# Performance work log

Hardware: AMD Instinct MI355X
Metric: run time of the kernel (lower is better)

## Reference

```python
import jax, jax.numpy as jnp
import numpy as np

WS = 8            # window_size
SHIFT = WS // 2   # cyclic shift
NHEADS = 6
EPS = 1e-5


def _rel_pos_index(ws):
    coords = np.stack(np.meshgrid(np.arange(ws), np.arange(ws), indexing='ij'))  # [2,ws,ws]
    flat = coords.reshape(2, -1)                       # [2,N]
    rel = flat[:, :, None] - flat[:, None, :]          # [2,N,N]
    rel = rel.transpose(1, 2, 0).copy()
    rel[:, :, 0] += ws - 1
    rel[:, :, 1] += ws - 1
    rel[:, :, 0] *= 2 * ws - 1
    return rel.sum(-1)                                 # [N,N] indices into bias table


def _attn_mask(H, W, ws, shift):
    # standard Swin boundary mask for the shifted configuration
    img = np.zeros((H, W))
    cnt = 0
    for hs in (slice(0, -ws), slice(-ws, -shift), slice(-shift, None)):
        for wsl in (slice(0, -ws), slice(-ws, -shift), slice(-shift, None)):
            img[hs, wsl] = cnt
            cnt += 1
    mw = img.reshape(H // ws, ws, W // ws, ws).transpose(0, 2, 1, 3).reshape(-1, ws * ws)
    m = mw[:, None, :] - mw[:, :, None]
    return np.where(m != 0, -100.0, 0.0).astype(np.float32)  # [nW, N, N]


def instance_norm(x):
    # InstanceNorm over spatial dims, no affine (torch default)
    m = x.mean(axis=(2, 3), keepdims=True)
    v = x.var(axis=(2, 3), keepdims=True)
    return (x - m) * jax.lax.rsqrt(v + EPS)


def setup_inputs() -> dict:
    key = jax.random.key(0)
    ks = jax.random.split(key, 8)
    B, C, H, W, E = 4, 192, 256, 256, 128
    s = 0.02
    return {
        'x': jax.random.normal(ks[0], (B, C, H, W), jnp.float32),
        'cond': jax.random.normal(ks[1], (B, E), jnp.float32),
        'qkv_w': jax.random.normal(ks[2], (3 * C, C), jnp.float32) * s,
        'qkv_b': jnp.zeros((3 * C,), jnp.float32),
        'proj_w': jax.random.normal(ks[3], (C, C), jnp.float32) * s,
        'proj_b': jnp.zeros((C,), jnp.float32),
        'rel_bias': jax.random.normal(ks[4], ((2 * WS - 1) ** 2, NHEADS), jnp.float32) * s,
        'film_w': jax.random.normal(ks[5], (2 * C, E), jnp.float32) * s,
        'film_b': jnp.zeros((2 * C,), jnp.float32),
    }


def shifted_window_attention(xn, qkv_w, qkv_b, proj_w, proj_b, rel_bias):
    B, C, H, W = xn.shape
    h, ws, shift = NHEADS, WS, SHIFT
    d = C // h
    N = ws * ws
    nW = (H // ws) * (W // ws)
    scale = d ** -0.5

    xs = jnp.transpose(xn, (0, 2, 3, 1))                         # BHWC
    xs = jnp.roll(xs, (-shift, -shift), axis=(1, 2))             # cyclic shift
    win = xs.reshape(B, H // ws, ws, W // ws, ws, C)
    win = win.transpose(0, 1, 3, 2, 4, 5).reshape(B * nW, N, C)  # window partition

    qkv = win @ qkv_w.T + qkv_b                                  # [Bn, N, 3C]
    q, k, v = [t.reshape(B * nW, N, h, d).transpose(0, 2, 1, 3)
               for t in jnp.split(qkv, 3, axis=-1)]              # [Bn, h, N, d]

    attn = jnp.einsum('bhnd,bhmd->bhnm', q, k) * scale           # [Bn, h, N, N]
    bias = rel_bias[_rel_pos_index(ws)].transpose(2, 0, 1)       # [h, N, N]
    attn = attn + bias[None]
    mask = jnp.asarray(_attn_mask(H, W, ws, shift))              # [nW, N, N]
    attn = attn.reshape(B, nW, h, N, N) + mask[None, :, None]
    attn = jax.nn.softmax(attn, axis=-1).reshape(B * nW, h, N, N)

    out = jnp.einsum('bhnm,bhmd->bhnd', attn, v)                 # [Bn, h, N, d]
    out = out.transpose(0, 2, 1, 3).reshape(B * nW, N, C)
    out = out @ proj_w.T + proj_b

    out = out.reshape(B, H // ws, W // ws, ws, ws, C)
    out = out.transpose(0, 1, 3, 2, 4, 5).reshape(B, H, W, C)    # window merge
    out = jnp.roll(out, (shift, shift), axis=(1, 2))             # reverse shift
    return jnp.transpose(out, (0, 3, 1, 2))                      # BCHW


def reference(x, cond, qkv_w, qkv_b, proj_w, proj_b, rel_bias, film_w, film_b):
    # branch 1: x + attn(norm1(x))
    xn = instance_norm(x)
    x = x + shifted_window_attention(xn, qkv_w, qkv_b, proj_w, proj_b, rel_bias)
    # branch 2: x + FiLM(norm2(x), cond)
    x2 = instance_norm(x)
    gb = cond @ film_w.T + film_b                                # [B, 2C]
    gamma, beta = jnp.split(gb, 2, axis=-1)
    x2 = x2 * gamma[:, :, None, None] + beta[:, :, None, None]
    return x + x2
```

## Files before the change

### kernel.cpp

```cpp
#include <hip/hip_runtime.h>

#define BATCH 4
#define CH    192
#define PLANE 65536

typedef unsigned short u16;
typedef unsigned char  u8;
typedef __bf16 bf16x8_t __attribute__((ext_vector_type(8)));
typedef unsigned short u16x8 __attribute__((ext_vector_type(8)));
typedef unsigned short u16x4 __attribute__((ext_vector_type(4)));
typedef float f32x4 __attribute__((ext_vector_type(4)));

__device__ __forceinline__ u16 f2bf(float f) {
  __bf16 h = (__bf16)f;
  return __builtin_bit_cast(u16, h);
}
__device__ __forceinline__ float bf2f(u16 h) {
  unsigned u = ((unsigned)h) << 16;
  return __builtin_bit_cast(float, u);
}
__device__ __forceinline__ f32x4 mfma16(u16x8 a, u16x8 b, f32x4 c) {
  return __builtin_amdgcn_mfma_f32_16x16x32_bf16(
      __builtin_bit_cast(bf16x8_t, a), __builtin_bit_cast(bf16x8_t, b), c, 0, 0, 0);
}

__global__ void stats_kernel(const float* __restrict__ in, float* __restrict__ st) {
  const int plane = blockIdx.x;
  const float4* p = (const float4*)(in + (long)plane * PLANE);
  float s = 0.f, ss = 0.f;
  for (int i = threadIdx.x; i < PLANE/4; i += 256) {
    float4 v = p[i];
    s  += v.x + v.y + v.z + v.w;
    ss += v.x*v.x + v.y*v.y + v.z*v.z + v.w*v.w;
  }
  for (int off = 1; off < 64; off <<= 1) {
    s  += __shfl_xor(s,  off, 64);
    ss += __shfl_xor(ss, off, 64);
  }
  __shared__ float aux[4][2];
  const int w = threadIdx.x >> 6;
  if ((threadIdx.x & 63) == 0) { aux[w][0] = s; aux[w][1] = ss; }
  __syncthreads();
  if (threadIdx.x == 0) {
    float S  = aux[0][0]+aux[1][0]+aux[2][0]+aux[3][0];
    float SS = aux[0][1]+aux[1][1]+aux[2][1]+aux[3][1];
    float mean = S * (1.f/PLANE);
    float var  = SS * (1.f/PLANE) - mean*mean;
    st[plane*2]   = mean;
    st[plane*2+1] = rsqrtf(var + 1e-5f);
  }
}

__global__ void cvt_kernel(const float* __restrict__ a, const float* __restrict__ b,
                           const float* __restrict__ rb,
                           u16* __restrict__ wa, u16* __restrict__ wb, u8* __restrict__ bq) {
  const int i = blockIdx.x*256 + threadIdx.x;
  if (i < 576*192) wa[i] = f2bf(a[i]);
  if (i < 192*192) wb[i] = f2bf(b[i]);
  if (i < 1350) {
    float v = fminf(fmaxf(rintf(rb[i]*128.f) + 128.f, 0.f), 255.f);
    bq[i] = (u8)v;
  }
}

__global__ void film_prep(const float* __restrict__ cond, const float* __restrict__ fw,
                          const float* __restrict__ fb, float* __restrict__ gb) {
  const int i = blockIdx.x*256 + threadIdx.x;
  if (i >= BATCH*384) return;
  const int bb = i / 384, oc = i - bb*384;
  const float* cw = fw + oc*128;
  const float* cv = cond + bb*128;
  float s = fb[oc];
  for (int k = 0; k < 128; ++k) s += cv[k]*cw[k];
  gb[i] = s;
}

__global__ __launch_bounds__(256) void prep_kernel(
    const float* __restrict__ x, const float* __restrict__ st, u16* __restrict__ xn)
{
  __shared__ u16 tile[32*264];
  const int t = threadIdx.x;
  const int bid = blockIdx.x;
  const int cc = bid % 6;
  const int wh = (bid/6) % 32;
  const int b  = bid / 192;
  const int c0 = cc*32;
  const int ww = t >> 3, ax = t & 7;
  const int gx = (ww*8 + ax + 4) & 255;
  const int gxb = gx & ~3, gxr = gx & 3;
  const long wid = b*1024 + wh*32 + ww;

  for (int ay = 0; ay < 8; ++ay) {
    const int gy = (wh*8 + ay + 4) & 255;
    for (int it = 0; it < 8; ++it) {
      const int id = it*256 + t;
      const int cl = id >> 6;
      const int px = (id & 63) << 2;
      const int c  = c0 + cl;
      const float m = st[(b*192+c)*2], r = st[(b*192+c)*2+1];
      float4 v = *(const float4*)(x + (((long)(b*192+c)) << 16) + gy*256 + px);
      u16x4 pk;
      pk[0] = f2bf((v.x-m)*r); pk[1] = f2bf((v.y-m)*r);
      pk[2] = f2bf((v.z-m)*r); pk[3] = f2bf((v.w-m)*r);
      *(u16x4*)&tile[cl*264 + (px ^ ((cl&7)<<2))] = pk;
    }
    __syncthreads();
    u16* dst = xn + wid*12288 + (ay*8+ax)*192 + c0;
    #pragma unroll
    for (int k = 0; k < 4; ++k) {
      u16x8 pk;
      #pragma unroll
      for (int e = 0; e < 8; ++e) {
        const int c = k*8 + e;
        pk[e] = tile[c*264 + (gxb ^ ((c&7)<<2)) + gxr];
      }
      *(u16x8*)(dst + k*8) = pk;
    }
    __syncthreads();
  }
}

__global__ __launch_bounds__(512, 4) void attn_kernel(
    const u16* __restrict__ xn, const u16* __restrict__ wq, const u16* __restrict__ wp,
    const float* __restrict__ qkvb, const float* __restrict__ projb,
    const u8* __restrict__ bq, const float* __restrict__ st,
    u16* __restrict__ pw, float2* __restrict__ part)
{
  __shared__ __attribute__((aligned(16))) unsigned char smem[71504];
  u16*    Xs    = (u16*)smem;
  u16*    G     = (u16*)(smem + 25600);
  u16*    Vt    = (u16*)(smem + 43008);
  u16*    Pout  = (u16*)(smem + 25600);
  u8*     biasQ = (u8*)(smem + 52224);
  float2* stp   = (float2*)(smem + 53576);
  u16*    Ps    = (u16*)(smem + 55120);

  const int t    = threadIdx.x;
  const int lane = t & 63;
  const int wave = t >> 6;
  const int arow = lane & 15;
  const int kgrp = lane >> 4;

  const int bid = blockIdx.x;
  const int wid = (bid & 7) * 512 + (bid >> 3);
  const int b   = wid >> 10;
  const int wh  = (wid >> 5) & 31;
  const int ww  = wid & 31;

  const u16* src = xn + (long)wid*12288;
  #pragma unroll
  for (int it = 0; it < 3; ++it) {
    const int id = it*512 + t;
    const int row = id/24, c8 = (id%24)*8;
    *(u16x8*)&Xs[row*200 + c8] = *(const u16x8*)(src + id*8);
  }
  for (int i = t; i < 1350; i += 512) biasQ[i] = bq[i];
  for (int i = t; i < 192; i += 512) {
    const float mean = st[(b*192+i)*2];
    const float rstd = st[(b*192+i)*2 + 1];
    float2 o = {mean, 1.0f / rstd};
    stp[i] = o;
  }
  __syncthreads();

  const int hh = wave >> 2;
  const int mt = wave & 3;
  const bool boundary = (wh == 31) || (ww == 31);
  u16x4 og[3][2];

  #pragma unroll
  for (int g = 0; g < 3; ++g) {
    for (int nt0 = wave; nt0 < 12; nt0 += 8) {
      f32x4 acc[4] = {{0,0,0,0},{0,0,0,0},{0,0,0,0},{0,0,0,0}};
      const int col = nt0*16 + arow;
      const int mat = col >> 6;
      const int ch  = mat*192 + g*64 + (col & 63);
      const u16* wrow = wq + ch*192 + kgrp*8;
      #pragma unroll
      for (int ks = 0; ks < 6; ++ks) {
        u16x8 bfr = *(const u16x8*)(wrow + ks*32);
        #pragma unroll
        for (int m = 0; m < 4; ++m) {
          u16x8 af = *(const u16x8*)&Xs[(m*16+arow)*200 + ks*32 + kgrp*8];
          acc[m] = mfma16(af, bfr, acc[m]);
        }
      }
      const float addb = qkvb[ch];
      if (mat == 2) {
        const int vc = col & 63;
        #pragma unroll
        for (int m = 0; m < 4; ++m) {
          u16x4 pk;
          #pragma unroll
          for (int r = 0; r < 4; ++r) pk[r] = f2bf(acc[m][r] + addb);
          *(u16x4*)&Vt[vc*72 + m*16 + kgrp*4] = pk;
        }
      } else {
        const float mult = (mat == 0) ? 0.17677669529663687f : 1.0f;
        const int gc = mat*64 + (col & 63);
        #pragma unroll
        for (int m = 0; m < 4; ++m)
          #pragma unroll
          for (int r = 0; r < 4; ++r)
            G[(m*16 + kgrp*4 + r)*136 + gc] = f2bf((acc[m][r] + addb)*mult);
      }
    }
    __syncthreads();

    const int hd = g*2 + hh;
    u16x8 qf = *(const u16x8*)&G[(mt*16+arow)*136 + hh*32 + kgrp*8];
    f32x4 sv[4];
    #pragma unroll
    for (int nt = 0; nt < 4; ++nt) {
      u16x8 kf = *(const u16x8*)&G[(nt*16+arow)*136 + 64 + hh*32 + kgrp*8];
      f32x4 z = {0,0,0,0};
      sv[nt] = mfma16(qf, kf, z);
    }

    int qj6[4];
    #pragma unroll
    for (int nt = 0; nt < 4; ++nt) {
      const int j = nt*16 + arow;
      qj6[nt] = ((j>>3)*15 + (j&7))*6;
    }
    float p[4][4];
    if (!boundary) {
      #pragma unroll
      for (int r = 0; r < 4; ++r) {
        const int i = mt*16 + kgrp*4 + r;
        const int qib = ((i>>3)*15 + (i&7) + 112)*6 + hd;
        #pragma unroll
        for (int nt = 0; nt < 4; ++nt)
          p[nt][r] = sv[nt][r] + (float)((int)biasQ[qib - qj6[nt]] - 128) * 0.0078125f;
      }
    } else {
      #pragma unroll
      for (int r = 0; r < 4; ++r) {
        const int i  = mt*16 + kgrp*4 + r;
        const int iy = i >> 3, ix = i & 7;
        const int qib = (iy*15 + ix + 112)*6 + hd;
        const int ri = ((wh==31) ? (iy<4?1:2) : 0)*3 + ((ww==31) ? (ix<4?1:2) : 0);
        #pragma unroll
        for (int nt = 0; nt < 4; ++nt) {
          const int j  = nt*16 + arow;
          const int jy = j >> 3, jx = j & 7;
          const int rj = ((wh==31) ? (jy<4?1:2) : 0)*3 + ((ww==31) ? (jx<4?1:2) : 0);
          float sc = sv[nt][r] + (float)((int)biasQ[qib - qj6[nt]] - 128) * 0.0078125f;
          if (ri != rj) sc -= 100.0f;
          p[nt][r] = sc;
        }
      }
    }
    #pragma unroll
    for (int r = 0; r < 4; ++r) {
      float mx = fmaxf(fmaxf(p[0][r], p[1][r]), fmaxf(p[2][r], p[3][r]));
      for (int off = 1; off < 16; off <<= 1) mx = fmaxf(mx, __shfl_xor(mx, off, 64));
      float sum = 0.f;
      #pragma unroll
      for (int nt = 0; nt < 4; ++nt) { p[nt][r] = __expf(p[nt][r] - mx); sum += p[nt][r]; }
      for (int off = 1; off < 16; off <<= 1) sum += __shfl_xor(sum, off, 64);
      const float inv = 1.0f / sum;
      #pragma unroll
      for (int nt = 0; nt < 4; ++nt) p[nt][r] *= inv;
    }
    u16* myP = Ps + wave*1024;
    #pragma unroll
    for (int r = 0; r < 4; ++r) {
      const int i = kgrp*4 + r;
      #pragma unroll
      for (int nt = 0; nt < 4; ++nt) {
        const int j = nt*16 + arow;
        myP[i*64 + ((j + 8*i) & 63)] = f2bf(p[nt][r]);
      }
    }
    f32x4 oacc[2] = {{0,0,0,0},{0,0,0,0}};
    #pragma unroll
    for (int ks = 0; ks < 2; ++ks) {
      u16x8 pf = *(const u16x8*)&myP[arow*64 + ((ks*32 + kgrp*8 + 8*arow) & 63)];
      #pragma unroll
      for (int nt = 0; nt < 2; ++nt) {
        u16x8 vf = *(const u16x8*)&Vt[(hh*32 + nt*16 + arow)*72 + ks*32 + kgrp*8];
        oacc[nt] = mfma16(pf, vf, oacc[nt]);
      }
    }
    #pragma unroll
    for (int nt = 0; nt < 2; ++nt)
      #pragma unroll
      for (int r = 0; r < 4; ++r)
        og[g][nt][r] = f2bf(oacc[nt][r]);
    __syncthreads();
  }

  u16x8 rawreg[3];
  #pragma unroll
  for (int it = 0; it < 3; ++it) {
    const int id = it*512 + t;
    const int c = id >> 3, tk8 = (id & 7)*8;
    const float2 mi = stp[c];
    u16x8 rr;
    #pragma unroll
    for (int e = 0; e < 8; ++e) {
      float nv = bf2f(Xs[(tk8 + e)*200 + c]);
      rr[e] = f2bf(nv*mi.y + mi.x);
    }
    rawreg[it] = rr;
  }
  __syncthreads();

  #pragma unroll
  for (int g = 0; g < 3; ++g)
    #pragma unroll
    for (int nt = 0; nt < 2; ++nt) {
      const int colb = g*64 + hh*32 + nt*16 + arow;
      #pragma unroll
      for (int r = 0; r < 4; ++r)
        Xs[(mt*16 + kgrp*4 + r)*200 + colb] = og[g][nt][r];
    }
  __syncthreads();

  for (int nt0 = wave; nt0 < 12; nt0 += 8) {
    const int ch = nt0*16 + arow;
    const float pb = projb[ch];
    f32x4 acc[4];
    #pragma unroll
    for (int m = 0; m < 4; ++m) { f32x4 v = {pb,pb,pb,pb}; acc[m] = v; }
    const u16* wrow = wp + ch*192 + kgrp*8;
    #pragma unroll
    for (int ks = 0; ks < 6; ++ks) {
      u16x8 bfr = *(const u16x8*)(wrow + ks*32);
      #pragma unroll
      for (int m = 0; m < 4; ++m) {
        u16x8 af = *(const u16x8*)&Xs[(m*16+arow)*200 + ks*32 + kgrp*8];
        acc[m] = mfma16(af, bfr, acc[m]);
      }
    }
    #pragma unroll
    for (int m = 0; m < 4; ++m) {
      u16x4 pk;
      #pragma unroll
      for (int r = 0; r < 4; ++r) pk[r] = f2bf(acc[m][r]);
      *(u16x4*)&Pout[ch*72 + m*16 + kgrp*4] = pk;
    }
  }
  __syncthreads();

  u16* dstw = pw + (long)wid*12288;
  #pragma unroll
  for (int it = 0; it < 3; ++it) {
    const int id = it*512 + t;
    const int c = id >> 3, tk8 = (id & 7)*8;
    u16x8 pv = *(const u16x8*)&Pout[c*72 + tk8];
    u16x8 rr = rawreg[it];
    u16x8 vb;
    float s = 0.f, q = 0.f;
    #pragma unroll
    for (int e = 0; e < 8; ++e) {
      float v = bf2f(rr[e]) + bf2f(pv[e]);
      vb[e] = f2bf(v);
      s += v; q += v*v;
    }
    *(u16x8*)(dstw + c*64 + tk8) = vb;
    s += __shfl_xor(s, 1, 64); q += __shfl_xor(q, 1, 64);
    s += __shfl_xor(s, 2, 64); q += __shfl_xor(q, 2, 64);
    s += __shfl_xor(s, 4, 64); q += __shfl_xor(q, 4, 64);
    if ((lane & 7) == 0) {
      float2 pr = {s, q};
      part[(long)wid*192 + c] = pr;
    }
  }
}

__global__ __launch_bounds__(256) void stats2_kernel(
    const float2* __restrict__ part, float2* __restrict__ st2f) {
  const int b = blockIdx.x / 12, cg = blockIdx.x % 12;
  const int cl = threadIdx.x & 15;
  const int w0 = threadIdx.x >> 4;
  const int c = cg*16 + cl;
  float s = 0.f, q = 0.f;
  for (int w = w0; w < 1024; w += 16) {
    float2 v = part[((long)(b*1024 + w))*192 + c];
    s += v.x; q += v.y;
  }
  s += __shfl_xor(s, 16, 64); q += __shfl_xor(q, 16, 64);
  s += __shfl_xor(s, 32, 64); q += __shfl_xor(q, 32, 64);
  __shared__ float2 aux[4][16];
  if ((threadIdx.x & 63) < 16) { float2 v = {s, q}; aux[threadIdx.x >> 6][cl] = v; }
  __syncthreads();
  if (threadIdx.x < 16) {
    float2 a0 = aux[0][cl], a1 = aux[1][cl], a2 = aux[2][cl], a3 = aux[3][cl];
    float S = a0.x + a1.x + a2.x + a3.x;
    float Q = a0.y + a1.y + a2.y + a3.y;
    float mean = S * (1.f/PLANE);
    float var  = Q * (1.f/PLANE) - mean*mean;
    float2 o = {mean, rsqrtf(var + 1e-5f)};
    st2f[b*192 + c] = o;
  }
}

__global__ __launch_bounds__(256) void final_kernel(
    const u16* __restrict__ pw, const float2* __restrict__ st2f,
    const float* __restrict__ gb, float* __restrict__ out)
{
  __shared__ u16 tile[32*264];
  const int t = threadIdx.x;
  const int bid = blockIdx.x;
  const int lin = (bid & 7)*768 + (bid >> 3);
  const int cc = lin % 6;
  const int rowid = lin / 6;
  const int gy = rowid & 255;
  const int b  = rowid >> 8;
  const int c0 = cc*32;
  const int gys = (gy + 252) & 255;
  const int wh = gys >> 3, ay = gys & 7;

  {
    const int ww = t >> 3, cq = t & 7;
    const long wid = b*1024 + wh*32 + ww;
    const u16* srcw = pw + wid*12288;
    const int g1 = ww*8 + 4, g2 = (ww*8 + 8) & 255;
    #pragma unroll
    for (int j = 0; j < 4; ++j) {
      const int c = cq*4 + j;
      u16x8 v = *(const u16x8*)(srcw + (c0+c)*64 + ay*8);
      const int sw = (c & 7) << 2;
      u16x4 lo = {v[0],v[1],v[2],v[3]}, hi = {v[4],v[5],v[6],v[7]};
      *(u16x4*)&tile[c*264 + (g1 ^ sw)] = lo;
      *(u16x4*)&tile[c*264 + (g2 ^ sw)] = hi;
    }
  }
  __syncthreads();

  const int cl = t >> 3, seg = t & 7;
  const int c = c0 + cl;
  const float2 mr = st2f[b*192 + c];
  const float mean = mr.x, rstd = mr.y;
  const float gmm  = gb[b*384 + c];
  const float be   = gb[b*384 + 192 + c];
  const long base = (((long)(b*192 + c)) << 16) + gy*256 + seg*32;
  float* orow = out + base;
  const int sw = (cl & 7) << 2;
  #pragma unroll
  for (int q4 = 0; q4 < 32; q4 += 4) {
    const int px = seg*32 + q4;
    u16x4 pv = *(const u16x4*)&tile[cl*264 + (px ^ sw)];
    float4 o;
    float v0 = bf2f(pv[0]), v1 = bf2f(pv[1]), v2 = bf2f(pv[2]), v3 = bf2f(pv[3]);
    o.x = v0 + (v0 - mean)*rstd*gmm + be;
    o.y = v1 + (v1 - mean)*rstd*gmm + be;
    o.z = v2 + (v2 - mean)*rstd*gmm + be;
    o.w = v3 + (v3 - mean)*rstd*gmm + be;
    *(float4*)(orow + q4) = o;
  }
}

extern "C" void kernel_launch(void* const* d_in, const int* in_sizes, int n_in,
                              void* d_out, int out_size, void* d_ws, size_t ws_size,
                              hipStream_t stream) {
  const float* x      = (const float*)d_in[0];
  const float* cond   = (const float*)d_in[1];
  const float* qkv_w  = (const float*)d_in[2];
  const float* qkv_b  = (const float*)d_in[3];
  const float* proj_w = (const float*)d_in[4];
  const float* proj_b = (const float*)d_in[5];
  const float* relb   = (const float*)d_in[6];
  const float* film_w = (const float*)d_in[7];
  const float* film_b = (const float*)d_in[8];
  float* out = (float*)d_out;

  char* ws = (char*)d_ws;
  float*  stats1 = (float*)ws;
  float2* st2f   = (float2*)(ws + 6144);
  float*  gb     = (float*)(ws + 12288);
  u16*    wq     = (u16*)(ws + 18432);
  u16*    wp     = (u16*)(ws + 239616);
  u8*     bqq    = (u8*)(ws + 313344);
  u16*    xbuf   = (u16*)(ws + 362496);
  float2* part   = (float2*)(ws + 362496 + 100663296);

  stats_kernel<<<768, 256, 0, stream>>>(x, stats1);
  cvt_kernel<<<432, 256, 0, stream>>>(qkv_w, proj_w, relb, wq, wp, bqq);
  film_prep<<<6, 256, 0, stream>>>(cond, film_w, film_b, gb);
  prep_kernel<<<768, 256, 0, stream>>>(x, stats1, xbuf);
  attn_kernel<<<4096, 512, 0, stream>>>(xbuf, wq, wp, qkv_b, proj_b, bqq, stats1, xbuf, part);
  stats2_kernel<<<48, 256, 0, stream>>>(part, st2f);
  final_kernel<<<6144, 256, 0, stream>>>(xbuf, st2f, gb, out);
}
```

Before: 505.7 us.

## Fuse first instance-norm stats into prep pass and normalize inside attention

```diff
diff --git a/kernel.cpp b/kernel.cpp
--- a/kernel.cpp
+++ b/kernel.cpp
@@ -22,33 +22,6 @@
 __device__ __forceinline__ f32x4 mfma16(u16x8 a, u16x8 b, f32x4 c) {
   return __builtin_amdgcn_mfma_f32_16x16x32_bf16(
       __builtin_bit_cast(bf16x8_t, a), __builtin_bit_cast(bf16x8_t, b), c, 0, 0, 0);
-}
-
-__global__ void stats_kernel(const float* __restrict__ in, float* __restrict__ st) {
-  const int plane = blockIdx.x;
-  const float4* p = (const float4*)(in + (long)plane * PLANE);
-  float s = 0.f, ss = 0.f;
-  for (int i = threadIdx.x; i < PLANE/4; i += 256) {
-    float4 v = p[i];
-    s  += v.x + v.y + v.z + v.w;
-    ss += v.x*v.x + v.y*v.y + v.z*v.z + v.w*v.w;
-  }
-  for (int off = 1; off < 64; off <<= 1) {
-    s  += __shfl_xor(s,  off, 64);
-    ss += __shfl_xor(ss, off, 64);
-  }
-  __shared__ float aux[4][2];
-  const int w = threadIdx.x >> 6;
-  if ((threadIdx.x & 63) == 0) { aux[w][0] = s; aux[w][1] = ss; }
-  __syncthreads();
-  if (threadIdx.x == 0) {
-    float S  = aux[0][0]+aux[1][0]+aux[2][0]+aux[3][0];
-    float SS = aux[0][1]+aux[1][1]+aux[2][1]+aux[3][1];
-    float mean = S * (1.f/PLANE);
-    float var  = SS * (1.f/PLANE) - mean*mean;
-    st[plane*2]   = mean;
-    st[plane*2+1] = rsqrtf(var + 1e-5f);
-  }
 }
 
 __global__ void cvt_kernel(const float* __restrict__ a, const float* __restrict__ b,
@@ -76,7 +49,7 @@
 }
 
 __global__ __launch_bounds__(256) void prep_kernel(
-    const float* __restrict__ x, const float* __restrict__ st, u16* __restrict__ xn)
+    const float* __restrict__ x, u16* __restrict__ xraw, float2* __restrict__ part1)
 {
   __shared__ u16 tile[32*264];
   const int t = threadIdx.x;
@@ -90,22 +63,33 @@
   const int gxb = gx & ~3, gxr = gx & 3;
   const long wid = b*1024 + wh*32 + ww;
 
+  const int scl = t >> 3, sseg = t & 7;
+  float myS = 0.f, myQ = 0.f;
+
   for (int ay = 0; ay < 8; ++ay) {
     const int gy = (wh*8 + ay + 4) & 255;
     for (int it = 0; it < 8; ++it) {
       const int id = it*256 + t;
       const int cl = id >> 6;
       const int px = (id & 63) << 2;
-      const int c  = c0 + cl;
-      const float m = st[(b*192+c)*2], r = st[(b*192+c)*2+1];
-      float4 v = *(const float4*)(x + (((long)(b*192+c)) << 16) + gy*256 + px);
+      float4 v = *(const float4*)(x + (((long)(b*192+c0+cl)) << 16) + gy*256 + px);
       u16x4 pk;
-      pk[0] = f2bf((v.x-m)*r); pk[1] = f2bf((v.y-m)*r);
-      pk[2] = f2bf((v.z-m)*r); pk[3] = f2bf((v.w-m)*r);
+      pk[0] = f2bf(v.x); pk[1] = f2bf(v.y); pk[2] = f2bf(v.z); pk[3] = f2bf(v.w);
       *(u16x4*)&tile[cl*264 + (px ^ ((cl&7)<<2))] = pk;
     }
     __syncthreads();
-    u16* dst = xn + wid*12288 + (ay*8+ax)*192 + c0;
+    {
+      const int sw = (scl & 7) << 2;
+      #pragma unroll
+      for (int k = 0; k < 32; k += 4) {
+        const int px = sseg*32 + k;
+        u16x4 pv = *(const u16x4*)&tile[scl*264 + (px ^ sw)];
+        float a0 = bf2f(pv[0]), a1 = bf2f(pv[1]), a2 = bf2f(pv[2]), a3 = bf2f(pv[3]);
+        myS += a0 + a1 + a2 + a3;
+        myQ += a0*a0 + a1*a1 + a2*a2 + a3*a3;
+      }
+    }
+    u16* dst = xraw + wid*12288 + (ay*8+ax)*192 + c0;
     #pragma unroll
     for (int k = 0; k < 4; ++k) {
       u16x8 pk;
@@ -118,6 +102,31 @@
     }
     __syncthreads();
   }
+  for (int off = 1; off < 8; off <<= 1) {
+    myS += __shfl_xor(myS, off, 64);
+    myQ += __shfl_xor(myQ, off, 64);
+  }
+  if (sseg == 0) {
+    float2 pr = {myS, myQ};
+    part1[((b*32 + wh)*6 + cc)*32 + scl] = pr;
+  }
+}
+
+__global__ __launch_bounds__(256) void statsR_kernel(
+    const float2* __restrict__ part1, float* __restrict__ st) {
+  const int i = blockIdx.x*256 + threadIdx.x;
+  if (i >= 768) return;
+  const int b = i / 192, c = i % 192;
+  const int cg = c >> 5, cl = c & 31;
+  float s = 0.f, q = 0.f;
+  for (int wh = 0; wh < 32; ++wh) {
+    float2 v = part1[((b*32 + wh)*6 + cg)*32 + cl];
+    s += v.x; q += v.y;
+  }
+  const float mean = s * (1.f/PLANE);
+  const float var  = q * (1.f/PLANE) - mean*mean;
+  st[i*2]   = mean;
+  st[i*2+1] = rsqrtf(var + 1e-5f);
 }
 
 __global__ __launch_bounds__(512, 4) void attn_kernel(
@@ -126,14 +135,15 @@
     const u8* __restrict__ bq, const float* __restrict__ st,
     u16* __restrict__ pw, float2* __restrict__ part)
 {
-  __shared__ __attribute__((aligned(16))) unsigned char smem[71504];
+  __shared__ __attribute__((aligned(16))) unsigned char smem[73040];
   u16*    Xs    = (u16*)smem;
   u16*    G     = (u16*)(smem + 25600);
   u16*    Vt    = (u16*)(smem + 43008);
   u16*    Pout  = (u16*)(smem + 25600);
   u8*     biasQ = (u8*)(smem + 52224);
-  float2* stp   = (float2*)(smem + 53576);
-  u16*    Ps    = (u16*)(smem + 55120);
+  float2* stpN  = (float2*)(smem + 53576);
+  float2* stpR  = (float2*)(smem + 55112);
+  u16*    Ps    = (u16*)(smem + 56656);
 
   const int t    = threadIdx.x;
   const int lane = t & 63;
@@ -147,19 +157,30 @@
   const int wh  = (wid >> 5) & 31;
   const int ww  = wid & 31;
 
+  for (int i = t; i < 1350; i += 512) biasQ[i] = bq[i];
+  if (t < 192) {
+    const float mean = st[(b*192 + t)*2];
+    const float rstd = st[(b*192 + t)*2 + 1];
+    float2 n = {mean, rstd};
+    float2 r = {mean, 1.0f / rstd};
+    stpN[t] = n;
+    stpR[t] = r;
+  }
+  __syncthreads();
+
   const u16* src = xn + (long)wid*12288;
   #pragma unroll
   for (int it = 0; it < 3; ++it) {
     const int id = it*512 + t;
     const int row = id/24, c8 = (id%24)*8;
-    *(u16x8*)&Xs[row*200 + c8] = *(const u16x8*)(src + id*8);
-  }
-  for (int i = t; i < 1350; i += 512) biasQ[i] = bq[i];
-  for (int i = t; i < 192; i += 512) {
-    const float mean = st[(b*192+i)*2];
-    const float rstd = st[(b*192+i)*2 + 1];
-    float2 o = {mean, 1.0f / rstd};
-    stp[i] = o;
+    u16x8 raw = *(const u16x8*)(src + id*8);
+    u16x8 nrm;
+    #pragma unroll
+    for (int e = 0; e < 8; ++e) {
+      float2 mr = stpN[c8 + e];
+      nrm[e] = f2bf((bf2f(raw[e]) - mr.x) * mr.y);
+    }
+    *(u16x8*)&Xs[row*200 + c8] = nrm;
   }
   __syncthreads();
 
@@ -296,7 +317,7 @@
   for (int it = 0; it < 3; ++it) {
     const int id = it*512 + t;
     const int c = id >> 3, tk8 = (id & 7)*8;
-    const float2 mi = stp[c];
+    const float2 mi = stpR[c];
     u16x8 rr;
     #pragma unroll
     for (int e = 0; e < 8; ++e) {
@@ -404,31 +425,17 @@
   __shared__ u16 tile[32*264];
   const int t = threadIdx.x;
   const int bid = blockIdx.x;
-  const int lin = (bid & 7)*768 + (bid >> 3);
+  const int lin = (bid & 7)*96 + (bid >> 3);
   const int cc = lin % 6;
-  const int rowid = lin / 6;
-  const int gy = rowid & 255;
-  const int b  = rowid >> 8;
+  const int band = lin / 6;
+  const int wh = band & 31;
+  const int b  = band >> 5;
   const int c0 = cc*32;
-  const int gys = (gy + 252) & 255;
-  const int wh = gys >> 3, ay = gys & 7;
-
-  {
-    const int ww = t >> 3, cq = t & 7;
-    const long wid = b*1024 + wh*32 + ww;
-    const u16* srcw = pw + wid*12288;
-    const int g1 = ww*8 + 4, g2 = (ww*8 + 8) & 255;
-    #pragma unroll
-    for (int j = 0; j < 4; ++j) {
-      const int c = cq*4 + j;
-      u16x8 v = *(const u16x8*)(srcw + (c0+c)*64 + ay*8);
-      const int sw = (c & 7) << 2;
-      u16x4 lo = {v[0],v[1],v[2],v[3]}, hi = {v[4],v[5],v[6],v[7]};
-      *(u16x4*)&tile[c*264 + (g1 ^ sw)] = lo;
-      *(u16x4*)&tile[c*264 + (g2 ^ sw)] = hi;
-    }
-  }
-  __syncthreads();
+
+  const int ww = t >> 3, cq = t & 7;
+  const long wid = b*1024 + wh*32 + ww;
+  const u16* srcw = pw + wid*12288;
+  const int g1 = ww*8 + 4, g2 = (ww*8 + 8) & 255;
 
   const int cl = t >> 3, seg = t & 7;
   const int c = c0 + cl;
@@ -436,20 +443,36 @@
   const float mean = mr.x, rstd = mr.y;
   const float gmm  = gb[b*384 + c];
   const float be   = gb[b*384 + 192 + c];
-  const long base = (((long)(b*192 + c)) << 16) + gy*256 + seg*32;
-  float* orow = out + base;
-  const int sw = (cl & 7) << 2;
-  #pragma unroll
-  for (int q4 = 0; q4 < 32; q4 += 4) {
-    const int px = seg*32 + q4;
-    u16x4 pv = *(const u16x4*)&tile[cl*264 + (px ^ sw)];
-    float4 o;
-    float v0 = bf2f(pv[0]), v1 = bf2f(pv[1]), v2 = bf2f(pv[2]), v3 = bf2f(pv[3]);
-    o.x = v0 + (v0 - mean)*rstd*gmm + be;
-    o.y = v1 + (v1 - mean)*rstd*gmm + be;
-    o.z = v2 + (v2 - mean)*rstd*gmm + be;
-    o.w = v3 + (v3 - mean)*rstd*gmm + be;
-    *(float4*)(orow + q4) = o;
+  const int swb = (cl & 7) << 2;
+
+  for (int ay = 0; ay < 8; ++ay) {
+    #pragma unroll
+    for (int j = 0; j < 4; ++j) {
+      const int ca = cq*4 + j;
+      u16x8 v = *(const u16x8*)(srcw + (c0+ca)*64 + ay*8);
+      const int sw = (ca & 7) << 2;
+      u16x4 lo = {v[0],v[1],v[2],v[3]}, hi = {v[4],v[5],v[6],v[7]};
+      *(u16x4*)&tile[ca*264 + (g1 ^ sw)] = lo;
+      *(u16x4*)&tile[ca*264 + (g2 ^ sw)] = hi;
+    }
+    __syncthreads();
+
+    const int gy = (wh*8 + ay + 4) & 255;
+    const long base = (((long)(b*192 + c)) << 16) + gy*256 + seg*32;
+    float* orow = out + base;
+    #pragma unroll
+    for (int q4 = 0; q4 < 32; q4 += 4) {
+      const int px = seg*32 + q4;
+      u16x4 pv = *(const u16x4*)&tile[cl*264 + (px ^ swb)];
+      float4 o;
+      float v0 = bf2f(pv[0]), v1 = bf2f(pv[1]), v2 = bf2f(pv[2]), v3 = bf2f(pv[3]);
+      o.x = v0 + (v0 - mean)*rstd*gmm + be;
+      o.y = v1 + (v1 - mean)*rstd*gmm + be;
+      o.z = v2 + (v2 - mean)*rstd*gmm + be;
+      o.w = v3 + (v3 - mean)*rstd*gmm + be;
+      *(float4*)(orow + q4) = o;
+    }
+    __syncthreads();
   }
 }
 
@@ -476,12 +499,13 @@
   u8*     bqq    = (u8*)(ws + 313344);
   u16*    xbuf   = (u16*)(ws + 362496);
   float2* part   = (float2*)(ws + 362496 + 100663296);
-
-  stats_kernel<<<768, 256, 0, stream>>>(x, stats1);
+  float2* part1  = (float2*)(ws + 362496 + 100663296 + 6291456);
+
   cvt_kernel<<<432, 256, 0, stream>>>(qkv_w, proj_w, relb, wq, wp, bqq);
   film_prep<<<6, 256, 0, stream>>>(cond, film_w, film_b, gb);
-  prep_kernel<<<768, 256, 0, stream>>>(x, stats1, xbuf);
+  prep_kernel<<<768, 256, 0, stream>>>(x, xbuf, part1);
+  statsR_kernel<<<3, 256, 0, stream>>>(part1, stats1);
   attn_kernel<<<4096, 512, 0, stream>>>(xbuf, wq, wp, qkv_b, proj_b, bqq, stats1, xbuf, part);
   stats2_kernel<<<48, 256, 0, stream>>>(part, st2f);
-  final_kernel<<<6144, 256, 0, stream>>>(xbuf, st2f, gb, out);
-}
+  final_kernel<<<768, 256, 0, stream>>>(xbuf, st2f, gb, out);
+}
```

Result: slower. 524.2 us (+3.7%).
